# Optimization experiments

Hardware: AMD Instinct MI355X
Metric: run time of the kernel (lower is better)

Reference implementation:

```python
import jax, jax.numpy as jnp
import numpy as np

B = 2048
T = 720
V = 64
K = 4
PHI_MAX = 0.25
N_KNOTS = 4


def setup_inputs() -> dict:
    key = jax.random.key(0)
    k1, k2, k3, k4 = jax.random.split(key, 4)
    y_hat = jax.random.normal(k1, (B, T, V), dtype=jnp.float32)
    # learned params (perturbed from the zero/one init so the edit is non-trivial)
    a = 0.1 * jax.random.normal(k2, (V, K), dtype=jnp.float32)
    phi = 0.1 * jax.random.normal(k3, (V, K), dtype=jnp.float32)
    env_knots = jax.random.uniform(k4, (V, N_KNOTS), dtype=jnp.float32, minval=0.5, maxval=1.5)
    k_bins = jnp.array([4, 30, 60, 120], dtype=jnp.int32)  # rFFT bin indices, < T//2+1
    return {"y_hat": y_hat, "a": a, "phi": phi, "env_knots": env_knots, "k_bins": k_bins}


def reference(y_hat, a, phi, env_knots, k_bins):
    Bn, Tn, Vn = y_hat.shape
    # full rFFT along time: [B, F, V] complex, F = T//2 + 1
    Fspec = jnp.fft.rfft(y_hat, n=Tn, axis=1)
    # per-(variable, bin) complex gain: (1 + a) * exp(i * tanh(phi) * phi_max)
    amp = 1.0 + a                               # [V, K]
    ph = jnp.tanh(phi) * PHI_MAX                # [V, K]
    scale = (amp * jnp.exp(1j * ph)).T          # [K, V] complex
    # edit only the seasonal bins (vectorized equivalent of the nested loops)
    Fspec = Fspec.at[:, k_bins, :].multiply(scale[None, :, :])
    y_corr = jnp.fft.irfft(Fspec, n=Tn, axis=1)  # [B, T, V] real
    # piecewise-linear envelope over [0, 1] with N_KNOTS control points
    t = jnp.linspace(0.0, 1.0, Tn)               # [T]
    pos = t * (N_KNOTS - 1)
    idx = jnp.clip(pos.astype(jnp.int32), 0, N_KNOTS - 2)  # [T]
    frac = pos - idx.astype(t.dtype)
    knots = jnp.clip(env_knots, 0.5, 1.5)        # [V, n_knots]
    env = knots[:, idx] * (1.0 - frac) + knots[:, idx + 1] * frac  # [V, T]
    return y_corr * env.T[None, :, :]
```

## Files before the change

kernel.cpp:

```cpp
#include <hip/hip_runtime.h>
#include <math.h>

#define T_LEN   720
#define V_DIM   64
#define KBINS   4
#define NKNOTS  4
#define BLOCK   768
#define TSLICE  15
#define NW      12
#define PIPE    4

#define WS_TAB  0
#define WS_SR   5760
#define WS_SI   6016
#define WS_KN   6272

__global__ __launch_bounds__(256) void precompute_kernel(
    const float* __restrict__ a, const float* __restrict__ phi,
    const float* __restrict__ env_knots, const int* __restrict__ k_bins,
    float* __restrict__ ws)
{
    int id = blockIdx.x * 256 + threadIdx.x;
    if (id < T_LEN * KBINS) {
        int t = id >> 2, k = id & 3;
        int kb = k_bins[k];
        int m  = (kb * t) % T_LEN;
        float th = (float)m * 0.00872664625997164788f;
        float sn, cs;
        sincosf(th, &sn, &cs);
        ws[WS_TAB + t * 8 + k]     = cs;
        ws[WS_TAB + t * 8 + 4 + k] = sn;
    } else if (id < T_LEN * KBINS + V_DIM * KBINS) {
        int e = id - T_LEN * KBINS;
        int v = e >> 2, k = e & 3;
        float amp = 1.0f + a[e];
        float ph  = tanhf(phi[e]) * 0.25f;
        float sp, cp;
        sincosf(ph, &sp, &cp);
        ws[WS_SR + k * V_DIM + v] = amp * cp - 1.0f;
        ws[WS_SI + k * V_DIM + v] = amp * sp;
    } else if (id < T_LEN * KBINS + V_DIM * KBINS + V_DIM * NKNOTS) {
        int e = id - T_LEN * KBINS - V_DIM * KBINS;
        int v = e >> 2, n = e & 3;
        ws[WS_KN + n * V_DIM + v] = fminf(fmaxf(env_knots[e], 0.5f), 1.5f);
    }
}

__global__ __launch_bounds__(BLOCK) void SeasonalEnvelopeAdapter_kernel(
    const float* __restrict__ y,
    const float* __restrict__ ws,
    float* __restrict__ out)
{
    __shared__ __align__(16) float tab[T_LEN * 8];
    __shared__ float red[16][NW][33];
    __shared__ __align__(16) float coefT[8][V_DIM];
    __shared__ __align__(16) float knT[NKNOTS][V_DIM];

    const int tid  = threadIdx.x;
    const int b    = blockIdx.x;
    const int g    = tid & 15;
    const int s    = tid >> 4;
    const int lane = tid & 63;
    const int w    = tid >> 6;

    for (int e = tid; e < 1440; e += BLOCK)
        ((float4*)tab)[e] = ((const float4*)(ws + WS_TAB))[e];
    if (tid < NKNOTS * V_DIM) ((float*)knT)[tid] = ws[WS_KN + tid];
    __syncthreads();

    const size_t base = (size_t)b * (T_LEN * V_DIM) + (size_t)(g << 2);
    float accre[4][4], accim[4][4];
    #pragma unroll
    for (int j = 0; j < 4; ++j)
        #pragma unroll
        for (int k = 0; k < 4; ++k) { accre[j][k] = 0.f; accim[j][k] = 0.f; }

    {
        float4 yv[PIPE];
        #pragma unroll
        for (int i0 = 0; i0 < PIPE; ++i0)
            yv[i0] = *(const float4*)(y + base + (size_t)(48 * i0 + s) * V_DIM);
        #pragma unroll
        for (int i = 0; i < TSLICE; ++i) {
            int t = 48 * i + s;
            float4 cur = yv[i & (PIPE - 1)];
            if (i + PIPE < TSLICE)
                yv[i & (PIPE - 1)] = *(const float4*)(y + base + (size_t)(48 * (i + PIPE) + s) * V_DIM);
            float4 c4 = *(const float4*)(&tab[t * 8]);
            float4 s4 = *(const float4*)(&tab[t * 8 + 4]);
            const float cs[4] = {c4.x, c4.y, c4.z, c4.w};
            const float sn[4] = {s4.x, s4.y, s4.z, s4.w};
            const float yj[4] = {cur.x, cur.y, cur.z, cur.w};
            #pragma unroll
            for (int j = 0; j < 4; ++j)
                #pragma unroll
                for (int k = 0; k < 4; ++k) {
                    accre[j][k] = fmaf(yj[j], cs[k], accre[j][k]);
                    accim[j][k] = fmaf(yj[j], sn[k], accim[j][k]);
                }
        }
    }

    #pragma unroll
    for (int j = 0; j < 4; ++j)
        #pragma unroll
        for (int k = 0; k < 4; ++k) {
            float r = accre[j][k], im = accim[j][k];
            r  += __shfl_xor(r, 16, 64);  r  += __shfl_xor(r, 32, 64);
            im += __shfl_xor(im, 16, 64); im += __shfl_xor(im, 32, 64);
            accre[j][k] = r; accim[j][k] = im;
        }
    if (lane < 16) {
        #pragma unroll
        for (int j = 0; j < 4; ++j)
            #pragma unroll
            for (int k = 0; k < 4; ++k) {
                red[lane][w][j * 8 + k]     = accre[j][k];
                red[lane][w][j * 8 + 4 + k] = accim[j][k];
            }
    }
    __syncthreads();

    if (tid < 256) {
        int v = tid >> 2, k = tid & 3;
        int gg = v >> 2, j = v & 3;
        float cr = 0.f, ci = 0.f;
        #pragma unroll
        for (int ww = 0; ww < NW; ++ww) {
            cr += red[gg][ww][j * 8 + k];
            ci += red[gg][ww][j * 8 + 4 + k];
        }
        float sr = ws[WS_SR + k * V_DIM + v];
        float si = ws[WS_SI + k * V_DIM + v];
        const float sc = 2.0f / (float)T_LEN;
        coefT[k][v]     = (cr * sr + ci * si) * sc;
        coefT[4 + k][v] = (cr * si - ci * sr) * sc;
    }
    __syncthreads();

    float cre[4][4], cim[4][4];
    #pragma unroll
    for (int k = 0; k < 4; ++k) {
        float4 r4 = *(const float4*)(&coefT[k][g << 2]);
        float4 i4 = *(const float4*)(&coefT[4 + k][g << 2]);
        cre[k][0] = r4.x; cre[k][1] = r4.y; cre[k][2] = r4.z; cre[k][3] = r4.w;
        cim[k][0] = i4.x; cim[k][1] = i4.y; cim[k][2] = i4.z; cim[k][3] = i4.w;
    }

    const float posScale = 3.0f / 719.0f;
    {
        float4 yv[PIPE];
        #pragma unroll
        for (int i0 = 0; i0 < PIPE; ++i0)
            yv[i0] = *(const float4*)(y + base + (size_t)(48 * i0 + s) * V_DIM);
        #pragma unroll
        for (int i = 0; i < TSLICE; ++i) {
            int t = 48 * i + s;
            float4 cur = yv[i & (PIPE - 1)];
            if (i + PIPE < TSLICE)
                yv[i & (PIPE - 1)] = *(const float4*)(y + base + (size_t)(48 * (i + PIPE) + s) * V_DIM);
            float4 c4 = *(const float4*)(&tab[t * 8]);
            float4 s4 = *(const float4*)(&tab[t * 8 + 4]);
            const float cs[4] = {c4.x, c4.y, c4.z, c4.w};
            const float sn[4] = {s4.x, s4.y, s4.z, s4.w};
            float pos = (float)t * posScale;
            int idx = (int)pos; idx = idx > 2 ? 2 : idx;
            float frac = pos - (float)idx;
            float4 e0v = *(const float4*)(&knT[idx][g << 2]);
            float4 e1v = *(const float4*)(&knT[idx + 1][g << 2]);
            const float e0[4] = {e0v.x, e0v.y, e0v.z, e0v.w};
            const float e1[4] = {e1v.x, e1v.y, e1v.z, e1v.w};
            const float yj[4] = {cur.x, cur.y, cur.z, cur.w};
            float oj[4];
            #pragma unroll
            for (int j = 0; j < 4; ++j) {
                float d = 0.f;
                #pragma unroll
                for (int k = 0; k < 4; ++k)
                    d = fmaf(cre[k][j], cs[k], fmaf(-cim[k][j], sn[k], d));
                float env = fmaf(e1[j] - e0[j], frac, e0[j]);
                oj[j] = (yj[j] + d) * env;
            }
            float4 o; o.x = oj[0]; o.y = oj[1]; o.z = oj[2]; o.w = oj[3];
            *(float4*)(out + base + (size_t)t * V_DIM) = o;
        }
    }
}

extern "C" void kernel_launch(void* const* d_in, const int* in_sizes, int n_in,
                              void* d_out, int out_size, void* d_ws, size_t ws_size,
                              hipStream_t stream) {
    const float* y         = (const float*)d_in[0];
    const float* a         = (const float*)d_in[1];
    const float* phi       = (const float*)d_in[2];
    const float* env_knots = (const float*)d_in[3];
    const int*   k_bins    = (const int*)d_in[4];
    float* out = (float*)d_out;
    float* ws  = (float*)d_ws;

    int B = in_sizes[0] / (T_LEN * V_DIM);
    int ids = T_LEN * KBINS + V_DIM * KBINS + V_DIM * NKNOTS;
    precompute_kernel<<<(ids + 255) / 256, 256, 0, stream>>>(a, phi, env_knots, k_bins, ws);
    SeasonalEnvelopeAdapter_kernel<<<B, BLOCK, 0, stream>>>(y, ws, out);
}
```

Baseline: 183.1 us.

## Software-pipeline projection and correction passes across batches in persistent blocks

Each block now handles four batch rows in sequence. The DFT projection of row c runs in the same loop as the correction and write pass of row c-1, so loads and FMAs from the two phases interleave, and the shared table is loaded once per four rows. The correction coefficients are held in registers packed as bf16 to cut register pressure. Stores are now nontemporal. The costs are a 4x smaller grid (512 blocks), an extra sync round per chunk, a shallower prefetch depth, and lower precision in the correction term.

Result: slower. 315.5 us (+72.3%).

```diff
diff --git a/kernel.cpp b/kernel.cpp
--- a/kernel.cpp
+++ b/kernel.cpp
@@ -8,12 +8,19 @@
 #define BLOCK   768
 #define TSLICE  15
 #define NW      12
-#define PIPE    4
+#define CHUNK   4
+
+typedef float vfloat4 __attribute__((ext_vector_type(4)));
 
 #define WS_TAB  0
 #define WS_SR   5760
 #define WS_SI   6016
 #define WS_KN   6272
+
+__device__ __forceinline__ unsigned f2bf_rne(float f) {
+    unsigned u = __float_as_uint(f);
+    return (u + 0x7FFFu + ((u >> 16) & 1u)) >> 16;
+}
 
 __global__ __launch_bounds__(256) void precompute_kernel(
     const float* __restrict__ a, const float* __restrict__ phi,
@@ -49,7 +56,8 @@
 __global__ __launch_bounds__(BLOCK) void SeasonalEnvelopeAdapter_kernel(
     const float* __restrict__ y,
     const float* __restrict__ ws,
-    float* __restrict__ out)
+    float* __restrict__ out,
+    int B)
 {
     __shared__ __align__(16) float tab[T_LEN * 8];
     __shared__ float red[16][NW][33];
@@ -57,7 +65,6 @@
     __shared__ __align__(16) float knT[NKNOTS][V_DIM];
 
     const int tid  = threadIdx.x;
-    const int b    = blockIdx.x;
     const int g    = tid & 15;
     const int s    = tid >> 4;
     const int lane = tid & 63;
@@ -68,122 +75,142 @@
     if (tid < NKNOTS * V_DIM) ((float*)knT)[tid] = ws[WS_KN + tid];
     __syncthreads();
 
-    const size_t base = (size_t)b * (T_LEN * V_DIM) + (size_t)(g << 2);
+    const int b0 = blockIdx.x * CHUNK;
+    const float posScale = 3.0f / 719.0f;
     float accre[4][4], accim[4][4];
-    #pragma unroll
-    for (int j = 0; j < 4; ++j)
-        #pragma unroll
-        for (int k = 0; k < 4; ++k) { accre[j][k] = 0.f; accim[j][k] = 0.f; }
-
-    {
-        float4 yv[PIPE];
-        #pragma unroll
-        for (int i0 = 0; i0 < PIPE; ++i0)
-            yv[i0] = *(const float4*)(y + base + (size_t)(48 * i0 + s) * V_DIM);
+
+    #pragma unroll 1
+    for (int c = 0; c <= CHUNK; ++c) {
+        const int bP1 = b0 + c;
+        const int bP2 = b0 + c - 1;
+        const bool doP1 = (c < CHUNK) && (bP1 < B);
+        const bool doP2 = (c > 0) && (bP2 < B);
+
+        const size_t base1 = (size_t)bP1 * (T_LEN * V_DIM) + (size_t)(g << 2);
+        const size_t base2 = (size_t)bP2 * (T_LEN * V_DIM) + (size_t)(g << 2);
+
+        unsigned cre01[4], cre23[4], cim01[4], cim23[4];
+        if (doP2) {
+            #pragma unroll
+            for (int k = 0; k < 4; ++k) {
+                float4 r4 = *(const float4*)(&coefT[k][g << 2]);
+                float4 i4 = *(const float4*)(&coefT[4 + k][g << 2]);
+                cre01[k] = f2bf_rne(r4.x) | (f2bf_rne(r4.y) << 16);
+                cre23[k] = f2bf_rne(r4.z) | (f2bf_rne(r4.w) << 16);
+                cim01[k] = f2bf_rne(i4.x) | (f2bf_rne(i4.y) << 16);
+                cim23[k] = f2bf_rne(i4.z) | (f2bf_rne(i4.w) << 16);
+            }
+        }
+        if (doP1) {
+            #pragma unroll
+            for (int j = 0; j < 4; ++j)
+                #pragma unroll
+                for (int k = 0; k < 4; ++k) { accre[j][k] = 0.f; accim[j][k] = 0.f; }
+        }
+
+        float4 yv[2], zv[2];
+        if (doP1) {
+            yv[0] = *(const float4*)(y + base1 + (size_t)s * V_DIM);
+            yv[1] = *(const float4*)(y + base1 + (size_t)(48 + s) * V_DIM);
+        }
+        if (doP2) {
+            zv[0] = *(const float4*)(y + base2 + (size_t)s * V_DIM);
+            zv[1] = *(const float4*)(y + base2 + (size_t)(48 + s) * V_DIM);
+        }
+
         #pragma unroll
         for (int i = 0; i < TSLICE; ++i) {
-            int t = 48 * i + s;
-            float4 cur = yv[i & (PIPE - 1)];
-            if (i + PIPE < TSLICE)
-                yv[i & (PIPE - 1)] = *(const float4*)(y + base + (size_t)(48 * (i + PIPE) + s) * V_DIM);
+            const int t = 48 * i + s;
             float4 c4 = *(const float4*)(&tab[t * 8]);
             float4 s4 = *(const float4*)(&tab[t * 8 + 4]);
             const float cs[4] = {c4.x, c4.y, c4.z, c4.w};
             const float sn[4] = {s4.x, s4.y, s4.z, s4.w};
-            const float yj[4] = {cur.x, cur.y, cur.z, cur.w};
+
+            if (doP1) {
+                float4 cur = yv[i & 1];
+                if (i + 2 < TSLICE)
+                    yv[i & 1] = *(const float4*)(y + base1 + (size_t)(48 * (i + 2) + s) * V_DIM);
+                const float yj[4] = {cur.x, cur.y, cur.z, cur.w};
+                #pragma unroll
+                for (int j = 0; j < 4; ++j)
+                    #pragma unroll
+                    for (int k = 0; k < 4; ++k) {
+                        accre[j][k] = fmaf(yj[j], cs[k], accre[j][k]);
+                        accim[j][k] = fmaf(yj[j], sn[k], accim[j][k]);
+                    }
+            }
+            if (doP2) {
+                float4 cur = zv[i & 1];
+                if (i + 2 < TSLICE)
+                    zv[i & 1] = *(const float4*)(y + base2 + (size_t)(48 * (i + 2) + s) * V_DIM);
+                float d0 = 0.f, d1 = 0.f, d2 = 0.f, d3 = 0.f;
+                #pragma unroll
+                for (int k = 0; k < 4; ++k) {
+                    float ck = cs[k], sk = sn[k];
+                    float r0 = __uint_as_float(cre01[k] << 16);
+                    float r1 = __uint_as_float(cre01[k] & 0xFFFF0000u);
+                    float r2 = __uint_as_float(cre23[k] << 16);
+                    float r3 = __uint_as_float(cre23[k] & 0xFFFF0000u);
+                    float i0 = __uint_as_float(cim01[k] << 16);
+                    float i1 = __uint_as_float(cim01[k] & 0xFFFF0000u);
+                    float i2 = __uint_as_float(cim23[k] << 16);
+                    float i3 = __uint_as_float(cim23[k] & 0xFFFF0000u);
+                    d0 = fmaf(r0, ck, fmaf(-i0, sk, d0));
+                    d1 = fmaf(r1, ck, fmaf(-i1, sk, d1));
+                    d2 = fmaf(r2, ck, fmaf(-i2, sk, d2));
+                    d3 = fmaf(r3, ck, fmaf(-i3, sk, d3));
+                }
+                float pos = (float)t * posScale;
+                int idx = (int)pos; idx = idx > 2 ? 2 : idx;
+                float frac = pos - (float)idx;
+                float4 e0v = *(const float4*)(&knT[idx][g << 2]);
+                float4 e1v = *(const float4*)(&knT[idx + 1][g << 2]);
+                vfloat4 o;
+                o.x = (cur.x + d0) * fmaf(e1v.x - e0v.x, frac, e0v.x);
+                o.y = (cur.y + d1) * fmaf(e1v.y - e0v.y, frac, e0v.y);
+                o.z = (cur.z + d2) * fmaf(e1v.z - e0v.z, frac, e0v.z);
+                o.w = (cur.w + d3) * fmaf(e1v.w - e0v.w, frac, e0v.w);
+                __builtin_nontemporal_store(o, (vfloat4*)(out + base2 + (size_t)t * V_DIM));
+            }
+        }
+
+        if (doP1) {
             #pragma unroll
             for (int j = 0; j < 4; ++j)
                 #pragma unroll
                 for (int k = 0; k < 4; ++k) {
-                    accre[j][k] = fmaf(yj[j], cs[k], accre[j][k]);
-                    accim[j][k] = fmaf(yj[j], sn[k], accim[j][k]);
+                    float r = accre[j][k], im = accim[j][k];
+                    r  += __shfl_xor(r, 16, 64);  r  += __shfl_xor(r, 32, 64);
+                    im += __shfl_xor(im, 16, 64); im += __shfl_xor(im, 32, 64);
+                    accre[j][k] = r; accim[j][k] = im;
                 }
-        }
-    }
-
-    #pragma unroll
-    for (int j = 0; j < 4; ++j)
-        #pragma unroll
-        for (int k = 0; k < 4; ++k) {
-            float r = accre[j][k], im = accim[j][k];
-            r  += __shfl_xor(r, 16, 64);  r  += __shfl_xor(r, 32, 64);
-            im += __shfl_xor(im, 16, 64); im += __shfl_xor(im, 32, 64);
-            accre[j][k] = r; accim[j][k] = im;
-        }
-    if (lane < 16) {
-        #pragma unroll
-        for (int j = 0; j < 4; ++j)
-            #pragma unroll
-            for (int k = 0; k < 4; ++k) {
-                red[lane][w][j * 8 + k]     = accre[j][k];
-                red[lane][w][j * 8 + 4 + k] = accim[j][k];
-            }
-    }
-    __syncthreads();
-
-    if (tid < 256) {
-        int v = tid >> 2, k = tid & 3;
-        int gg = v >> 2, j = v & 3;
-        float cr = 0.f, ci = 0.f;
-        #pragma unroll
-        for (int ww = 0; ww < NW; ++ww) {
-            cr += red[gg][ww][j * 8 + k];
-            ci += red[gg][ww][j * 8 + 4 + k];
-        }
-        float sr = ws[WS_SR + k * V_DIM + v];
-        float si = ws[WS_SI + k * V_DIM + v];
-        const float sc = 2.0f / (float)T_LEN;
-        coefT[k][v]     = (cr * sr + ci * si) * sc;
-        coefT[4 + k][v] = (cr * si - ci * sr) * sc;
-    }
-    __syncthreads();
-
-    float cre[4][4], cim[4][4];
-    #pragma unroll
-    for (int k = 0; k < 4; ++k) {
-        float4 r4 = *(const float4*)(&coefT[k][g << 2]);
-        float4 i4 = *(const float4*)(&coefT[4 + k][g << 2]);
-        cre[k][0] = r4.x; cre[k][1] = r4.y; cre[k][2] = r4.z; cre[k][3] = r4.w;
-        cim[k][0] = i4.x; cim[k][1] = i4.y; cim[k][2] = i4.z; cim[k][3] = i4.w;
-    }
-
-    const float posScale = 3.0f / 719.0f;
-    {
-        float4 yv[PIPE];
-        #pragma unroll
-        for (int i0 = 0; i0 < PIPE; ++i0)
-            yv[i0] = *(const float4*)(y + base + (size_t)(48 * i0 + s) * V_DIM);
-        #pragma unroll
-        for (int i = 0; i < TSLICE; ++i) {
-            int t = 48 * i + s;
-            float4 cur = yv[i & (PIPE - 1)];
-            if (i + PIPE < TSLICE)
-                yv[i & (PIPE - 1)] = *(const float4*)(y + base + (size_t)(48 * (i + PIPE) + s) * V_DIM);
-            float4 c4 = *(const float4*)(&tab[t * 8]);
-            float4 s4 = *(const float4*)(&tab[t * 8 + 4]);
-            const float cs[4] = {c4.x, c4.y, c4.z, c4.w};
-            const float sn[4] = {s4.x, s4.y, s4.z, s4.w};
-            float pos = (float)t * posScale;
-            int idx = (int)pos; idx = idx > 2 ? 2 : idx;
-            float frac = pos - (float)idx;
-            float4 e0v = *(const float4*)(&knT[idx][g << 2]);
-            float4 e1v = *(const float4*)(&knT[idx + 1][g << 2]);
-            const float e0[4] = {e0v.x, e0v.y, e0v.z, e0v.w};
-            const float e1[4] = {e1v.x, e1v.y, e1v.z, e1v.w};
-            const float yj[4] = {cur.x, cur.y, cur.z, cur.w};
-            float oj[4];
-            #pragma unroll
-            for (int j = 0; j < 4; ++j) {
-                float d = 0.f;
-                #pragma unroll
-                for (int k = 0; k < 4; ++k)
-                    d = fmaf(cre[k][j], cs[k], fmaf(-cim[k][j], sn[k], d));
-                float env = fmaf(e1[j] - e0[j], frac, e0[j]);
-                oj[j] = (yj[j] + d) * env;
-            }
-            float4 o; o.x = oj[0]; o.y = oj[1]; o.z = oj[2]; o.w = oj[3];
-            *(float4*)(out + base + (size_t)t * V_DIM) = o;
-        }
+            if (lane < 16) {
+                #pragma unroll
+                for (int j = 0; j < 4; ++j)
+                    #pragma unroll
+                    for (int k = 0; k < 4; ++k) {
+                        red[lane][w][j * 8 + k]     = accre[j][k];
+                        red[lane][w][j * 8 + 4 + k] = accim[j][k];
+                    }
+            }
+        }
+        __syncthreads();
+        if (doP1 && tid < 256) {
+            int v = tid >> 2, k = tid & 3;
+            int gg = v >> 2, j = v & 3;
+            float cr = 0.f, ci = 0.f;
+            #pragma unroll
+            for (int ww = 0; ww < NW; ++ww) {
+                cr += red[gg][ww][j * 8 + k];
+                ci += red[gg][ww][j * 8 + 4 + k];
+            }
+            float sr = ws[WS_SR + k * V_DIM + v];
+            float si = ws[WS_SI + k * V_DIM + v];
+            const float sc = 2.0f / (float)T_LEN;
+            coefT[k][v]     = (cr * sr + ci * si) * sc;
+            coefT[4 + k][v] = (cr * si - ci * sr) * sc;
+        }
+        __syncthreads();
     }
 }
 
@@ -201,5 +228,6 @@
     int B = in_sizes[0] / (T_LEN * V_DIM);
     int ids = T_LEN * KBINS + V_DIM * KBINS + V_DIM * NKNOTS;
     precompute_kernel<<<(ids + 255) / 256, 256, 0, stream>>>(a, phi, env_knots, k_bins, ws);
-    SeasonalEnvelopeAdapter_kernel<<<B, BLOCK, 0, stream>>>(y, ws, out);
-}
+    int grid = (B + CHUNK - 1) / CHUNK;
+    SeasonalEnvelopeAdapter_kernel<<<grid, BLOCK, 0, stream>>>(y, ws, out, B);
+}
```

## Process multiple batches per block with cross-batch prefetch and nontemporal stores

Applied to the files above, without the earlier changes.

Each block now loops over eight batch rows instead of one, so the twiddle table load into shared memory is paid once per eight batches. During the second pass of one batch it prefetches the first rows of the next batch, overlapping the load latency across the two phases. Output writes become nontemporal stores to avoid polluting cache. The grid shrinks to 256 blocks on a device with many CUs, which risks underfilling the GPU, and the persistent loop adds register pressure.

After: 221.9 us. 1.21x slower.

```diff
diff --git a/kernel.cpp b/kernel.cpp
--- a/kernel.cpp
+++ b/kernel.cpp
@@ -8,7 +8,11 @@
 #define BLOCK   768
 #define TSLICE  15
 #define NW      12
-#define PIPE    4
+#define CHUNK   8
+#define P1P     4
+#define P2P     3
+
+typedef float vfloat4 __attribute__((ext_vector_type(4)));
 
 #define WS_TAB  0
 #define WS_SR   5760
@@ -49,7 +53,8 @@
 __global__ __launch_bounds__(BLOCK) void SeasonalEnvelopeAdapter_kernel(
     const float* __restrict__ y,
     const float* __restrict__ ws,
-    float* __restrict__ out)
+    float* __restrict__ out,
+    int B)
 {
     __shared__ __align__(16) float tab[T_LEN * 8];
     __shared__ float red[16][NW][33];
@@ -57,7 +62,6 @@
     __shared__ __align__(16) float knT[NKNOTS][V_DIM];
 
     const int tid  = threadIdx.x;
-    const int b    = blockIdx.x;
     const int g    = tid & 15;
     const int s    = tid >> 4;
     const int lane = tid & 63;
@@ -68,24 +72,38 @@
     if (tid < NKNOTS * V_DIM) ((float*)knT)[tid] = ws[WS_KN + tid];
     __syncthreads();
 
-    const size_t base = (size_t)b * (T_LEN * V_DIM) + (size_t)(g << 2);
-    float accre[4][4], accim[4][4];
-    #pragma unroll
-    for (int j = 0; j < 4; ++j)
-        #pragma unroll
-        for (int k = 0; k < 4; ++k) { accre[j][k] = 0.f; accim[j][k] = 0.f; }
-
-    {
-        float4 yv[PIPE];
-        #pragma unroll
-        for (int i0 = 0; i0 < PIPE; ++i0)
-            yv[i0] = *(const float4*)(y + base + (size_t)(48 * i0 + s) * V_DIM);
+    const int b0 = blockIdx.x * CHUNK;
+    const size_t vg = (size_t)(g << 2);
+    const float posScale = 3.0f / 719.0f;
+
+    float4 yv[P1P];
+    if (b0 < B) {
+        const size_t base0 = (size_t)b0 * (T_LEN * V_DIM) + vg;
+        #pragma unroll
+        for (int i0 = 0; i0 < P1P; ++i0)
+            yv[i0] = *(const float4*)(y + base0 + (size_t)(48 * i0 + s) * V_DIM);
+    }
+
+    #pragma unroll 1
+    for (int c = 0; c < CHUNK; ++c) {
+        const int b = b0 + c;
+        if (b >= B) break;
+        const size_t base  = (size_t)b * (T_LEN * V_DIM) + vg;
+        const bool pf = (c + 1 < CHUNK) && (b + 1 < B);
+        const size_t baseN = (size_t)(b + 1) * (T_LEN * V_DIM) + vg;
+
+        float accre[4][4], accim[4][4];
+        #pragma unroll
+        for (int j = 0; j < 4; ++j)
+            #pragma unroll
+            for (int k = 0; k < 4; ++k) { accre[j][k] = 0.f; accim[j][k] = 0.f; }
+
         #pragma unroll
         for (int i = 0; i < TSLICE; ++i) {
-            int t = 48 * i + s;
-            float4 cur = yv[i & (PIPE - 1)];
-            if (i + PIPE < TSLICE)
-                yv[i & (PIPE - 1)] = *(const float4*)(y + base + (size_t)(48 * (i + PIPE) + s) * V_DIM);
+            const int t = 48 * i + s;
+            float4 cur = yv[i & 3];
+            if (i + P1P < TSLICE)
+                yv[i & 3] = *(const float4*)(y + base + (size_t)(48 * (i + P1P) + s) * V_DIM);
             float4 c4 = *(const float4*)(&tab[t * 8]);
             float4 s4 = *(const float4*)(&tab[t * 8 + 4]);
             const float cs[4] = {c4.x, c4.y, c4.z, c4.w};
@@ -99,66 +117,64 @@
                     accim[j][k] = fmaf(yj[j], sn[k], accim[j][k]);
                 }
         }
-    }
-
-    #pragma unroll
-    for (int j = 0; j < 4; ++j)
+
+        #pragma unroll
+        for (int j = 0; j < 4; ++j)
+            #pragma unroll
+            for (int k = 0; k < 4; ++k) {
+                float r = accre[j][k], im = accim[j][k];
+                r  += __shfl_xor(r, 16, 64);  r  += __shfl_xor(r, 32, 64);
+                im += __shfl_xor(im, 16, 64); im += __shfl_xor(im, 32, 64);
+                accre[j][k] = r; accim[j][k] = im;
+            }
+        if (lane < 16) {
+            #pragma unroll
+            for (int j = 0; j < 4; ++j)
+                #pragma unroll
+                for (int k = 0; k < 4; ++k) {
+                    red[lane][w][j * 8 + k]     = accre[j][k];
+                    red[lane][w][j * 8 + 4 + k] = accim[j][k];
+                }
+        }
+        __syncthreads();
+        if (tid < 256) {
+            int v = tid >> 2, k = tid & 3;
+            int gg = v >> 2, j = v & 3;
+            float cr = 0.f, ci = 0.f;
+            #pragma unroll
+            for (int ww = 0; ww < NW; ++ww) {
+                cr += red[gg][ww][j * 8 + k];
+                ci += red[gg][ww][j * 8 + 4 + k];
+            }
+            float sr = ws[WS_SR + k * V_DIM + v];
+            float si = ws[WS_SI + k * V_DIM + v];
+            const float sc = 2.0f / (float)T_LEN;
+            coefT[k][v]     = (cr * sr + ci * si) * sc;
+            coefT[4 + k][v] = (cr * si - ci * sr) * sc;
+        }
+        __syncthreads();
+
+        float cre[4][4], cim[4][4];
         #pragma unroll
         for (int k = 0; k < 4; ++k) {
-            float r = accre[j][k], im = accim[j][k];
-            r  += __shfl_xor(r, 16, 64);  r  += __shfl_xor(r, 32, 64);
-            im += __shfl_xor(im, 16, 64); im += __shfl_xor(im, 32, 64);
-            accre[j][k] = r; accim[j][k] = im;
-        }
-    if (lane < 16) {
-        #pragma unroll
-        for (int j = 0; j < 4; ++j)
-            #pragma unroll
-            for (int k = 0; k < 4; ++k) {
-                red[lane][w][j * 8 + k]     = accre[j][k];
-                red[lane][w][j * 8 + 4 + k] = accim[j][k];
-            }
-    }
-    __syncthreads();
-
-    if (tid < 256) {
-        int v = tid >> 2, k = tid & 3;
-        int gg = v >> 2, j = v & 3;
-        float cr = 0.f, ci = 0.f;
-        #pragma unroll
-        for (int ww = 0; ww < NW; ++ww) {
-            cr += red[gg][ww][j * 8 + k];
-            ci += red[gg][ww][j * 8 + 4 + k];
-        }
-        float sr = ws[WS_SR + k * V_DIM + v];
-        float si = ws[WS_SI + k * V_DIM + v];
-        const float sc = 2.0f / (float)T_LEN;
-        coefT[k][v]     = (cr * sr + ci * si) * sc;
-        coefT[4 + k][v] = (cr * si - ci * sr) * sc;
-    }
-    __syncthreads();
-
-    float cre[4][4], cim[4][4];
-    #pragma unroll
-    for (int k = 0; k < 4; ++k) {
-        float4 r4 = *(const float4*)(&coefT[k][g << 2]);
-        float4 i4 = *(const float4*)(&coefT[4 + k][g << 2]);
-        cre[k][0] = r4.x; cre[k][1] = r4.y; cre[k][2] = r4.z; cre[k][3] = r4.w;
-        cim[k][0] = i4.x; cim[k][1] = i4.y; cim[k][2] = i4.z; cim[k][3] = i4.w;
-    }
-
-    const float posScale = 3.0f / 719.0f;
-    {
-        float4 yv[PIPE];
-        #pragma unroll
-        for (int i0 = 0; i0 < PIPE; ++i0)
-            yv[i0] = *(const float4*)(y + base + (size_t)(48 * i0 + s) * V_DIM);
+            float4 r4 = *(const float4*)(&coefT[k][g << 2]);
+            float4 i4 = *(const float4*)(&coefT[4 + k][g << 2]);
+            cre[k][0] = r4.x; cre[k][1] = r4.y; cre[k][2] = r4.z; cre[k][3] = r4.w;
+            cim[k][0] = i4.x; cim[k][1] = i4.y; cim[k][2] = i4.z; cim[k][3] = i4.w;
+        }
+        float4 zv[P2P];
+        #pragma unroll
+        for (int i0 = 0; i0 < P2P; ++i0)
+            zv[i0] = *(const float4*)(y + base + (size_t)(48 * i0 + s) * V_DIM);
+
         #pragma unroll
         for (int i = 0; i < TSLICE; ++i) {
-            int t = 48 * i + s;
-            float4 cur = yv[i & (PIPE - 1)];
-            if (i + PIPE < TSLICE)
-                yv[i & (PIPE - 1)] = *(const float4*)(y + base + (size_t)(48 * (i + PIPE) + s) * V_DIM);
+            const int t = 48 * i + s;
+            if (pf && i < P1P)
+                yv[i] = *(const float4*)(y + baseN + (size_t)(48 * i + s) * V_DIM);
+            float4 cur = zv[i % P2P];
+            if (i + P2P < TSLICE)
+                zv[i % P2P] = *(const float4*)(y + base + (size_t)(48 * (i + P2P) + s) * V_DIM);
             float4 c4 = *(const float4*)(&tab[t * 8]);
             float4 s4 = *(const float4*)(&tab[t * 8 + 4]);
             const float cs[4] = {c4.x, c4.y, c4.z, c4.w};
@@ -171,7 +187,7 @@
             const float e0[4] = {e0v.x, e0v.y, e0v.z, e0v.w};
             const float e1[4] = {e1v.x, e1v.y, e1v.z, e1v.w};
             const float yj[4] = {cur.x, cur.y, cur.z, cur.w};
-            float oj[4];
+            vfloat4 o;
             #pragma unroll
             for (int j = 0; j < 4; ++j) {
                 float d = 0.f;
@@ -179,10 +195,9 @@
                 for (int k = 0; k < 4; ++k)
                     d = fmaf(cre[k][j], cs[k], fmaf(-cim[k][j], sn[k], d));
                 float env = fmaf(e1[j] - e0[j], frac, e0[j]);
-                oj[j] = (yj[j] + d) * env;
+                o[j] = (yj[j] + d) * env;
             }
-            float4 o; o.x = oj[0]; o.y = oj[1]; o.z = oj[2]; o.w = oj[3];
-            *(float4*)(out + base + (size_t)t * V_DIM) = o;
+            __builtin_nontemporal_store(o, (vfloat4*)(out + base + (size_t)t * V_DIM));
         }
     }
 }
@@ -201,5 +216,6 @@
     int B = in_sizes[0] / (T_LEN * V_DIM);
     int ids = T_LEN * KBINS + V_DIM * KBINS + V_DIM * NKNOTS;
     precompute_kernel<<<(ids + 255) / 256, 256, 0, stream>>>(a, phi, env_knots, k_bins, ws);
-    SeasonalEnvelopeAdapter_kernel<<<B, BLOCK, 0, stream>>>(y, ws, out);
+    int grid = (B + CHUNK - 1) / CHUNK;
+    SeasonalEnvelopeAdapter_kernel<<<grid, BLOCK, 0, stream>>>(y, ws, out, B);
 }
```
